# Kernel optimization log

Measured on AMD Instinct MI355X. Metric: run time of the kernel, lower is better.

## Reference

```python
import jax, jax.numpy as jnp
import numpy as np

N, H, DDE, NH = 256, 256, 64, 4

def setup_inputs() -> dict:
    key = jax.random.key(0)
    ks = jax.random.split(key, 12)
    rn = lambda k, s, sc=1.0: (jax.random.normal(k, s) * sc).astype(jnp.float32)
    return {
        "action_hidden_state": rn(ks[0], (N, H)),
        "goal_hidden_state": rn(ks[1], (N, H)),
        "goal": rn(ks[2], (N, 2)),
        "action": rn(ks[3], (N, 2)),
        "W_dist": rn(ks[4], (8, DDE), 0.3),          # distEmbedding Linear(8, dde)
        "b_dist": jnp.zeros((DDE,), jnp.float32),
        "W_gate": rn(ks[5], (DDE, H), 0.1),          # gateFC Linear(dde, H)
        "b_gate": jnp.zeros((H,), jnp.float32),
        "w": rn(ks[6], (NH, 1, H, H), 0.06),         # GAT per-head projection
        "a": rn(ks[7], (1, 1, 2 * H, 1), 0.06),      # attention vector
        "bias": jnp.zeros((H,), jnp.float32),
    }

def reference(action_hidden_state, goal_hidden_state, goal, action,
              W_dist, b_dist, W_gate, b_gate, w, a, bias):
    n = goal.shape[0]
    # --- InteractionGate.cal_gate: x1[i,j] = x[j], x2[i,j] = x[i] ---
    g1 = jnp.broadcast_to(goal[None, :, :], (n, n, 2))
    g2 = jnp.broadcast_to(goal[:, None, :], (n, n, 2))
    a1 = jnp.broadcast_to(action[None, :, :], (n, n, 2))
    a2 = jnp.broadcast_to(action[:, None, :], (n, n, 2))
    dist = jnp.concatenate([a2, g2, a1, g1], axis=-1)                 # [n,n,8]
    gate = jax.nn.sigmoid(jax.nn.relu(dist @ W_dist + b_dist) @ W_gate + b_gate)  # [n,n,H]
    # temp_action_1[i,j] = action_hidden_state[j]
    gate_action = gate * jnp.tanh(action_hidden_state[None, :, :])    # [n,n,H]
    # diagonal entries replaced by goal_hidden_state (mask_goal = eye)
    eye = jnp.eye(n, dtype=bool)[:, :, None]
    gated_h = jnp.where(eye, goal_hidden_state[None, :, :], gate_action)  # [n,n,H]

    # --- GAT assembly: h_self[i,k] = ahs[i]; h_other = cat(ahs, gated_h) ---
    h_other = jnp.concatenate([action_hidden_state[:, None, :], gated_h], axis=1)  # [n,n+1,H]

    wm = w[:, 0]          # [NH,H,H]
    a_flat = a[0, 0, :, 0]  # [2H]
    f = wm.shape[-1]
    n_head = wm.shape[0]
    # h_self rows along k are all identical -> project once per (head, node)
    hsp = jnp.einsum('nh,zhf->znf', action_hidden_state, wm)          # [NH,n,f]
    hop = jnp.einsum('nkh,zhf->znkf', h_other, wm)                    # [NH,n,n+1,f]
    # cat([h_self', h_other']) @ a  ==  h_self'@a[:f] + h_other'@a[f:]
    score = (hsp @ a_flat[:f])[:, :, None] + hop @ a_flat[f:]         # [NH,n,n+1]
    e = jnp.where(score > 0, score, 0.2 * score)                      # LeakyReLU(0.2)
    alpha = jax.nn.softmax(e, axis=-1)                                # softmax over neighbors
    # h_attn = matmul(h_other, w) == hop; weighted sum over k, mean over heads
    out = jnp.einsum('znk,znkf->nf', alpha, hop) / n_head             # [n,f]
    return jax.nn.relu(out) + bias
```

## Files before the change

### kernel.cpp

```cpp
#include <hip/hip_runtime.h>
#include <hip/hip_bf16.h>

#define NN 256
#define HH 256

typedef __attribute__((ext_vector_type(8))) short short8;
typedef __attribute__((ext_vector_type(4))) float f32x4;

__device__ __forceinline__ ushort f2bf(float x) {
    __hip_bfloat16 h = __float2bfloat16(x);
    return *reinterpret_cast<ushort*>(&h);
}
__device__ __forceinline__ float bf2f(ushort u) {
    __hip_bfloat16 h = *reinterpret_cast<__hip_bfloat16*>(&u);
    return __bfloat162float(h);
}
__device__ __forceinline__ float fast_rcp(float x) {
    return __builtin_amdgcn_rcpf(x);
}
__device__ __forceinline__ float fast_tanh(float x) {
    float e = __expf(2.0f * x);
    return 1.0f - 2.0f * fast_rcp(e + 1.0f);
}
template <int CTRL>
__device__ __forceinline__ float dpp_add(float x) {
    int y = __builtin_amdgcn_update_dpp(0, __float_as_int(x), CTRL, 0xF, 0xF, true);
    return x + __int_as_float(y);
}
template <int CTRL>
__device__ __forceinline__ float dpp_max(float x) {
    int y = __builtin_amdgcn_update_dpp(0, __float_as_int(x), CTRL, 0xF, 0xF, true);
    return fmaxf(x, __int_as_float(y));
}
__device__ __forceinline__ float red16(float v) {
    v = dpp_add<0xB1>(v); v = dpp_add<0x4E>(v);
    v = dpp_add<0x141>(v); v = dpp_add<0x140>(v);
    return v;
}
__device__ __forceinline__ float red16max(float v) {
    v = dpp_max<0xB1>(v); v = dpp_max<0x4E>(v);
    v = dpp_max<0x141>(v); v = dpp_max<0x140>(v);
    return v;
}

#define WS_P   0
#define WS_Q   16384
#define WS_T   32768
#define WS_WA  98304
#define WS_WB  99328
#define WS_WGT 100352
#define WS_PV  108544
#define WS_ML  632832
#define WS_W2H 636928
#define WS_W2L 768000

__global__ __launch_bounds__(256) void precompute_kernel(
    const float* __restrict__ ahs, const float* __restrict__ goal,
    const float* __restrict__ action, const float* __restrict__ Wd,
    const float* __restrict__ b_dist, const float* __restrict__ Wg,
    const float* __restrict__ w, const float* __restrict__ a,
    float* __restrict__ ws)
{
    const int b = blockIdx.x;
    const int t = threadIdx.x;
    const int wid  = t >> 6;
    const int lane = t & 63;
    float* P  = ws + WS_P;
    float* Q  = ws + WS_Q;
    float* T  = ws + WS_T;
    float* WA = ws + WS_WA;
    float* WB = ws + WS_WB;
    ushort* WgT  = (ushort*)(ws + WS_WGT);
    ushort* W2hi = (ushort*)(ws + WS_W2H);
    ushort* W2lo = (ushort*)(ws + WS_W2L);

    __shared__ __align__(16) float tile[64][65];

    if (b < 16) {
        const int z  = b >> 2;
        const int rg = b & 3;
        const int hbase = rg*64 + wid*16;
        const f32x4 aB = *(const f32x4*)(a + lane*4);
        const f32x4 aA = *(const f32x4*)(a + HH + lane*4);
#pragma unroll 4
        for (int rr = 0; rr < 16; ++rr) {
            const int h = hbase + rr;
            const f32x4 w4 = *(const f32x4*)(w + z*HH*HH + h*HH + lane*4);
            float dA = w4.x*aA.x + w4.y*aA.y + w4.z*aA.z + w4.w*aA.w;
            float dB = w4.x*aB.x + w4.y*aB.y + w4.z*aB.z + w4.w*aB.w;
#pragma unroll
            for (int off = 32; off; off >>= 1) {
                dA += __shfl_xor(dA, off);
                dB += __shfl_xor(dB, off);
            }
            if (lane == 0) { WA[z*HH + h] = dA; WB[z*HH + h] = dB; }
        }
    } else if (b < 80) {
        const int idx = b - 16;
        const int k0  = (idx >> 2) * 64;
        const int f0  = (idx & 3) * 64;
        const int ff  = t & 63;
#pragma unroll 4
        for (int i = 0; i < 16; ++i) {
            const int kk = i*4 + wid;
            tile[kk][ff] = w[(k0 + kk)*HH + f0 + ff];
        }
        __syncthreads();
#pragma unroll 4
        for (int i = 0; i < 16; ++i) {
            const int fl = i*4 + wid;
            float x = tile[ff][fl];
            ushort hi = f2bf(x);
            ushort lo = f2bf(x - bf2f(hi));
            W2hi[(size_t)(f0 + fl)*1024 + k0 + ff] = hi;
            W2lo[(size_t)(f0 + fl)*1024 + k0 + ff] = lo;
        }
    } else if (b < 144) {
        const int i = (b - 80)*4 + wid;
        const int d = lane;
        float a0 = action[2*i], a1 = action[2*i+1];
        float g0 = goal[2*i],   g1 = goal[2*i+1];
        P[i*64 + d] = a0*Wd[0*64+d] + a1*Wd[1*64+d]
                    + g0*Wd[2*64+d] + g1*Wd[3*64+d] + b_dist[d];
        Q[i*64 + d] = a0*Wd[4*64+d] + a1*Wd[5*64+d]
                    + g0*Wd[6*64+d] + g1*Wd[7*64+d];
    } else if (b < 208) {
        const int d = b - 144;
        WgT[t*64 + d] = f2bf(Wg[d*HH + t]);
    } else {
        const int idx = ((b - 208)*256 + t)*4;
        float4 v = *(const float4*)(ahs + idx);
        float4 o;
        o.x = fast_tanh(v.x); o.y = fast_tanh(v.y);
        o.z = fast_tanh(v.z); o.w = fast_tanh(v.w);
        *(float4*)(T + idx) = o;
    }
}

__global__ __launch_bounds__(256, 2) void gat_partial_kernel(
    const float* __restrict__ ahs, const float* __restrict__ ghs,
    const float* __restrict__ b_gate, float* __restrict__ ws)
{
    const int n    = blockIdx.x >> 1;
    const int hh   = blockIdx.x & 1;
    const int t    = threadIdx.x;
    const int wid  = t >> 6;
    const int lane = t & 63;
    const int quad = lane >> 4;
    const int l15  = lane & 15;
    const int zg   = quad;
    const int jj   = l15;
    const int n0   = wid * 64;

    const float* P  = ws + WS_P;
    const float* Q  = ws + WS_Q;
    const float* T  = ws + WS_T;
    const float* WA = ws + WS_WA;
    const float* WB = ws + WS_WB;
    const ushort* WgT = (const ushort*)(ws + WS_WGT);
    float* PV = ws + WS_PV;
    float* ML = ws + WS_ML;

    __shared__ __align__(16) float part[2][4][16][4];
    __shared__ __align__(16) float alpha_w[4][16][4];
    __shared__ __align__(16) float vred[16][260];
    __shared__ __align__(16) ushort A_l[128*64];

    int hcol[4];
#pragma unroll
    for (int nt = 0; nt < 4; ++nt) hcol[nt] = n0 + nt*16 + l15;

    short8 bfrag[4][2];
    float  wa_reg[4][4];
    float  bgv[4], gval[4];
#pragma unroll
    for (int nt = 0; nt < 4; ++nt) {
#pragma unroll
        for (int kh = 0; kh < 2; ++kh)
            bfrag[nt][kh] = *(const short8*)(WgT + hcol[nt]*64 + kh*32 + quad*8);
#pragma unroll
        for (int z = 0; z < 4; ++z) wa_reg[z][nt] = WA[z*HH + hcol[nt]];
        bgv[nt]  = b_gate[hcol[nt]];
        gval[nt] = ghs[n*HH + hcol[nt]];
    }

    {
        const int jl = t >> 1;
        const int kh = t & 1;
        const float* prow = P + n*64 + kh*32;
        const float* qrow = Q + (hh*128 + jl)*64 + kh*32;
        ushort hv[32];
#pragma unroll
        for (int c = 0; c < 8; ++c) {
            f32x4 pq = *(const f32x4*)(prow + c*4);
            f32x4 qq = *(const f32x4*)(qrow + c*4);
            hv[c*4+0] = f2bf(fmaxf(pq.x + qq.x, 0.f));
            hv[c*4+1] = f2bf(fmaxf(pq.y + qq.y, 0.f));
            hv[c*4+2] = f2bf(fmaxf(pq.z + qq.z, 0.f));
            hv[c*4+3] = f2bf(fmaxf(pq.w + qq.w, 0.f));
        }
        char* rb = (char*)A_l + jl*128;
        const int sw = (jl & 7) << 4;
#pragma unroll
        for (int c2 = 0; c2 < 4; ++c2) {
            const int off = (kh*64 + c2*16) ^ sw;
            *(short8*)(rb + off) = *(const short8*)(hv + c2*8);
        }
    }

    float vacc[4][4];
    {
        float av[4];
#pragma unroll
        for (int nt = 0; nt < 4; ++nt) av[nt] = ahs[n*HH + hcol[nt]];
#pragma unroll
        for (int z = 0; z < 4; ++z)
#pragma unroll
            for (int nt = 0; nt < 4; ++nt)
                vacc[z][nt] = (hh == 0 && quad == 0) ? av[nt] : 0.f;
    }

    float cz_r, m_r, l_r;
    {
        float pc = 0.f, ps = 0.f;
        const int hb = jj*16;
#pragma unroll
        for (int i4 = 0; i4 < 4; ++i4) {
            f32x4 av = *(const f32x4*)(ahs + n*HH + hb + i4*4);
            f32x4 wb = *(const f32x4*)(WB + zg*HH + hb + i4*4);
            f32x4 wa = *(const f32x4*)(WA + zg*HH + hb + i4*4);
            pc = fmaf(av.x, wb.x, pc); pc = fmaf(av.y, wb.y, pc);
            pc = fmaf(av.z, wb.z, pc); pc = fmaf(av.w, wb.w, pc);
            ps = fmaf(av.x, wa.x, ps); ps = fmaf(av.y, wa.y, ps);
            ps = fmaf(av.z, wa.z, ps); ps = fmaf(av.w, wa.w, ps);
        }
        pc = red16(pc); ps = red16(ps);
        cz_r = pc;
        if (hh == 0) {
            float sc = pc + ps;
            m_r = sc > 0.f ? sc : 0.2f * sc;
            l_r = 1.0f;
        } else {
            m_r = -__builtin_inff();
            l_r = 0.0f;
        }
    }

    __syncthreads();

    float tval[4][4];
    {
        const int j0 = hh*128;
#pragma unroll
        for (int r = 0; r < 4; ++r) {
            const int jg = j0 + quad*4 + r;
#pragma unroll
            for (int nt = 0; nt < 4; ++nt)
                tval[nt][r] = T[jg*HH + hcol[nt]];
        }
    }

    for (int cc = 0; cc < 8; ++cc) {
        const int j0  = hh*128 + cc*16;
        const int par = cc & 1;

        const int jl = cc*16 + l15;
        const char* rb = (const char*)A_l + jl*128;
        const int sw = (l15 & 7) << 4;
        short8 afrag0 = *(const short8*)(rb + ((quad*16) ^ sw));
        short8 afrag1 = *(const short8*)(rb + ((64 + quad*16) ^ sw));

        f32x4 acc[4];
#pragma unroll
        for (int nt = 0; nt < 4; ++nt) {
            f32x4 a4 = (f32x4){0.f,0.f,0.f,0.f};
            a4 = __builtin_amdgcn_mfma_f32_16x16x32_bf16(afrag0, bfrag[nt][0], a4, 0, 0, 0);
            a4 = __builtin_amdgcn_mfma_f32_16x16x32_bf16(afrag1, bfrag[nt][1], a4, 0, 0, 0);
            acc[nt] = a4;
        }

        float vals[4][4];
#pragma unroll
        for (int r = 0; r < 4; ++r) {
            const int jg = j0 + quad*4 + r;
            const bool diag = (jg == n);
#pragma unroll
            for (int nt = 0; nt < 4; ++nt) {
                float u = acc[nt][r] + bgv[nt];
                float g = fast_rcp(1.0f + __expf(-u));
                vals[nt][r] = diag ? gval[nt] : g * tval[nt][r];
            }
        }

#pragma unroll
        for (int z = 0; z < 4; ++z) {
            float pp[4];
#pragma unroll
            for (int r = 0; r < 4; ++r) {
                float s = 0.f;
#pragma unroll
                for (int nt = 0; nt < 4; ++nt)
                    s = fmaf(vals[nt][r], wa_reg[z][nt], s);
                pp[r] = red16(s);
            }
            if (l15 == z) {
#pragma unroll
                for (int r = 0; r < 4; ++r)
                    part[par][z][quad*4 + r][wid] = pp[r];
            }
        }
        __syncthreads();

        float tnext[4][4];
        if (cc < 7) {
            const int j1 = j0 + 16;
#pragma unroll
            for (int r = 0; r < 4; ++r) {
                const int jg = j1 + quad*4 + r;
#pragma unroll
                for (int nt = 0; nt < 4; ++nt)
                    tnext[nt][r] = T[jg*HH + hcol[nt]];
            }
        }

        float scl0, scl1, scl2, scl3;
        {
            f32x4 pr = *(const f32x4*)&part[par][zg][jj][0];
            float s = cz_r + ((pr.x + pr.y) + (pr.z + pr.w));
            float e = s > 0.f ? s : 0.2f * s;
            float mx = red16max(e);
            float m_new = fmaxf(m_r, mx);
            float at = __expf(e - m_new);
            float ss = red16(at);
            float scale = __expf(m_r - m_new);
            l_r = l_r * scale + ss;
            m_r = m_new;
            alpha_w[wid][jj][zg] = at;
            scl0 = __shfl(scale, 0);
            scl1 = __shfl(scale, 16);
            scl2 = __shfl(scale, 32);
            scl3 = __shfl(scale, 48);
        }
#pragma unroll
        for (int nt = 0; nt < 4; ++nt) {
            vacc[0][nt] *= scl0; vacc[1][nt] *= scl1;
            vacc[2][nt] *= scl2; vacc[3][nt] *= scl3;
        }
#pragma unroll
        for (int r = 0; r < 4; ++r) {
            f32x4 al = *(const f32x4*)&alpha_w[wid][quad*4 + r][0];
#pragma unroll
            for (int nt = 0; nt < 4; ++nt) {
                float v = vals[nt][r];
                vacc[0][nt] = fmaf(al.x, v, vacc[0][nt]);
                vacc[1][nt] = fmaf(al.y, v, vacc[1][nt]);
                vacc[2][nt] = fmaf(al.z, v, vacc[2][nt]);
                vacc[3][nt] = fmaf(al.w, v, vacc[3][nt]);
            }
        }
        if (cc < 7) {
#pragma unroll
            for (int nt = 0; nt < 4; ++nt)
#pragma unroll
                for (int r = 0; r < 4; ++r)
                    tval[nt][r] = tnext[nt][r];
        }
    }

#pragma unroll
    for (int z = 0; z < 4; ++z)
#pragma unroll
        for (int nt = 0; nt < 4; ++nt)
            vred[quad*4 + z][hcol[nt]] = vacc[z][nt];
    __syncthreads();
#pragma unroll
    for (int z = 0; z < 4; ++z) {
        float s = (vred[0*4+z][t] + vred[1*4+z][t]) + (vred[2*4+z][t] + vred[3*4+z][t]);
        PV[((size_t)(hh*4 + z)*NN + n)*HH + t] = s;
    }
    if (wid == 0 && l15 == 0) {
        ML[((hh*4 + zg)*NN + n)*2 + 0] = m_r;
        ML[((hh*4 + zg)*NN + n)*2 + 1] = l_r;
    }
}

__global__ __launch_bounds__(256) void gat_out_kernel(
    const float* __restrict__ bias, const float* __restrict__ ws,
    float* __restrict__ out)
{
    const int n0 = (blockIdx.x >> 4) * 16;
    const int f0 = (blockIdx.x & 15) * 16;
    const int t    = threadIdx.x;
    const int wid  = t >> 6;
    const int lane = t & 63;
    const int quad = lane >> 4;
    const int l15  = lane & 15;

    const float* PV = ws + WS_PV;
    const float* ML = ws + WS_ML;
    const ushort* W2hi = (const ushort*)(ws + WS_W2H);
    const ushort* W2lo = (const ushort*)(ws + WS_W2L);

    __shared__ __align__(16) float redc[3][16][17];
    __shared__ __align__(16) float sq[16][4][2];

    if (t < 128) {
        const int n_i = t >> 3, z = (t >> 1) & 3, q = t & 1;
        float m = ML[((q*4 + z)*NN + n0 + n_i)*2 + 0];
        float l = ML[((q*4 + z)*NN + n0 + n_i)*2 + 1];
        float mm = fmaxf(m, __shfl_xor(m, 1));
        float s  = __expf(m - mm);
        float ls = l * s;
        ls += __shfl_xor(ls, 1);
        sq[n_i][z][q] = s * fast_rcp(ls);
    }
    __syncthreads();

    f32x4 acc = (f32x4){0.f,0.f,0.f,0.f};

    const float s0 = sq[l15][wid][0];
    const float s1 = sq[l15][wid][1];
    const float* pv0 = PV + ((size_t)(0*4 + wid)*NN + n0 + l15)*HH;
    const float* pv1 = PV + ((size_t)(1*4 + wid)*NN + n0 + l15)*HH;

    for (int ks = 0; ks < 8; ++ks) {
        const int kp = ks*32 + quad*8;
        f32x4 p0a = *(const f32x4*)(pv0 + kp);
        f32x4 p0b = *(const f32x4*)(pv0 + kp + 4);
        f32x4 p1a = *(const f32x4*)(pv1 + kp);
        f32x4 p1b = *(const f32x4*)(pv1 + kp + 4);
        float v[8];
        v[0] = s0*p0a.x + s1*p1a.x; v[1] = s0*p0a.y + s1*p1a.y;
        v[2] = s0*p0a.z + s1*p1a.z; v[3] = s0*p0a.w + s1*p1a.w;
        v[4] = s0*p0b.x + s1*p1b.x; v[5] = s0*p0b.y + s1*p1b.y;
        v[6] = s0*p0b.z + s1*p1b.z; v[7] = s0*p0b.w + s1*p1b.w;
        ushort hi[8], lo[8];
#pragma unroll
        for (int c = 0; c < 8; ++c) {
            hi[c] = f2bf(v[c]);
            lo[c] = f2bf(v[c] - bf2f(hi[c]));
        }
        short8 ah = *(short8*)hi;
        short8 al = *(short8*)lo;
        const size_t boff = (size_t)(f0 + l15)*1024 + wid*256 + kp;
        short8 bh = *(const short8*)(W2hi + boff);
        short8 bl = *(const short8*)(W2lo + boff);
        acc = __builtin_amdgcn_mfma_f32_16x16x32_bf16(ah, bh, acc, 0, 0, 0);
        acc = __builtin_amdgcn_mfma_f32_16x16x32_bf16(ah, bl, acc, 0, 0, 0);
        acc = __builtin_amdgcn_mfma_f32_16x16x32_bf16(al, bh, acc, 0, 0, 0);
    }

    if (wid > 0) {
#pragma unroll
        for (int r = 0; r < 4; ++r)
            redc[wid-1][quad*4 + r][l15] = acc[r];
    }
    __syncthreads();
    if (wid == 0) {
        const int f = f0 + l15;
        float bv = bias[f];
#pragma unroll
        for (int r = 0; r < 4; ++r) {
            const int row = quad*4 + r;
            float s = acc[r]
                    + redc[0][row][l15]
                    + redc[1][row][l15]
                    + redc[2][row][l15];
            out[(size_t)(n0 + row)*HH + f] = fmaxf(0.25f * s, 0.f) + bv;
        }
    }
}

extern "C" void kernel_launch(void* const* d_in, const int* in_sizes, int n_in,
                              void* d_out, int out_size, void* d_ws, size_t ws_size,
                              hipStream_t stream)
{
    const float* ahs    = (const float*)d_in[0];
    const float* ghs    = (const float*)d_in[1];
    const float* goal   = (const float*)d_in[2];
    const float* action = (const float*)d_in[3];
    const float* Wd     = (const float*)d_in[4];
    const float* b_dist = (const float*)d_in[5];
    const float* Wg     = (const float*)d_in[6];
    const float* b_gate = (const float*)d_in[7];
    const float* w      = (const float*)d_in[8];
    const float* a      = (const float*)d_in[9];
    const float* bias   = (const float*)d_in[10];
    float* ws   = (float*)d_ws;
    float* outp = (float*)d_out;

    precompute_kernel<<<272, 256, 0, stream>>>(ahs, goal, action, Wd, b_dist, Wg, w, a, ws);
    gat_partial_kernel<<<512, 256, 0, stream>>>(ahs, ghs, b_gate, ws);
    gat_out_kernel<<<256, 256, 0, stream>>>(bias, ws, outp);
}
```

Measured before the change: 114.6 us.

## Split GAT partial work into four neighbor quarters per node

Each node's neighbor range is now split into four blocks of 64 instead of two blocks of 128, doubling the grid to 1024 blocks and raising the launch-bounds occupancy hint to 4. The output kernel merges four partial softmax states (max/sum) and four partial PV sums instead of two. The aim is more parallelism and better latency hiding across the MI355X CUs. In exchange the workspace for partial PV doubles, the output kernel reads twice as much partial data, and the higher occupancy target may force register spilling.

```diff
diff --git a/kernel.cpp b/kernel.cpp
--- a/kernel.cpp
+++ b/kernel.cpp
@@ -50,9 +50,9 @@
 #define WS_WB  99328
 #define WS_WGT 100352
 #define WS_PV  108544
-#define WS_ML  632832
-#define WS_W2H 636928
-#define WS_W2L 768000
+#define WS_ML  1157120
+#define WS_W2H 1165312
+#define WS_W2L 1296384
 
 __global__ __launch_bounds__(256) void precompute_kernel(
     const float* __restrict__ ahs, const float* __restrict__ goal,
@@ -137,12 +137,12 @@
     }
 }
 
-__global__ __launch_bounds__(256, 2) void gat_partial_kernel(
+__global__ __launch_bounds__(256, 4) void gat_partial_kernel(
     const float* __restrict__ ahs, const float* __restrict__ ghs,
     const float* __restrict__ b_gate, float* __restrict__ ws)
 {
-    const int n    = blockIdx.x >> 1;
-    const int hh   = blockIdx.x & 1;
+    const int n    = blockIdx.x >> 2;
+    const int qq   = blockIdx.x & 3;
     const int t    = threadIdx.x;
     const int wid  = t >> 6;
     const int lane = t & 63;
@@ -164,7 +164,7 @@
     __shared__ __align__(16) float part[2][4][16][4];
     __shared__ __align__(16) float alpha_w[4][16][4];
     __shared__ __align__(16) float vred[16][260];
-    __shared__ __align__(16) ushort A_l[128*64];
+    __shared__ __align__(16) ushort A_l[64*64];
 
     int hcol[4];
 #pragma unroll
@@ -185,25 +185,25 @@
     }
 
     {
-        const int jl = t >> 1;
-        const int kh = t & 1;
-        const float* prow = P + n*64 + kh*32;
-        const float* qrow = Q + (hh*128 + jl)*64 + kh*32;
-        ushort hv[32];
-#pragma unroll
-        for (int c = 0; c < 8; ++c) {
+        const int jl   = t >> 2;
+        const int kseg = t & 3;
+        const float* prow = P + n*64 + kseg*16;
+        const float* qrow = Q + (qq*64 + jl)*64 + kseg*16;
+        ushort hv[16];
+#pragma unroll
+        for (int c = 0; c < 4; ++c) {
             f32x4 pq = *(const f32x4*)(prow + c*4);
-            f32x4 qq = *(const f32x4*)(qrow + c*4);
-            hv[c*4+0] = f2bf(fmaxf(pq.x + qq.x, 0.f));
-            hv[c*4+1] = f2bf(fmaxf(pq.y + qq.y, 0.f));
-            hv[c*4+2] = f2bf(fmaxf(pq.z + qq.z, 0.f));
-            hv[c*4+3] = f2bf(fmaxf(pq.w + qq.w, 0.f));
+            f32x4 qv = *(const f32x4*)(qrow + c*4);
+            hv[c*4+0] = f2bf(fmaxf(pq.x + qv.x, 0.f));
+            hv[c*4+1] = f2bf(fmaxf(pq.y + qv.y, 0.f));
+            hv[c*4+2] = f2bf(fmaxf(pq.z + qv.z, 0.f));
+            hv[c*4+3] = f2bf(fmaxf(pq.w + qv.w, 0.f));
         }
         char* rb = (char*)A_l + jl*128;
         const int sw = (jl & 7) << 4;
 #pragma unroll
-        for (int c2 = 0; c2 < 4; ++c2) {
-            const int off = (kh*64 + c2*16) ^ sw;
+        for (int c2 = 0; c2 < 2; ++c2) {
+            const int off = (kseg*32 + c2*16) ^ sw;
             *(short8*)(rb + off) = *(const short8*)(hv + c2*8);
         }
     }
@@ -217,7 +217,7 @@
         for (int z = 0; z < 4; ++z)
 #pragma unroll
             for (int nt = 0; nt < 4; ++nt)
-                vacc[z][nt] = (hh == 0 && quad == 0) ? av[nt] : 0.f;
+                vacc[z][nt] = (qq == 0 && quad == 0) ? av[nt] : 0.f;
     }
 
     float cz_r, m_r, l_r;
@@ -236,7 +236,7 @@
         }
         pc = red16(pc); ps = red16(ps);
         cz_r = pc;
-        if (hh == 0) {
+        if (qq == 0) {
             float sc = pc + ps;
             m_r = sc > 0.f ? sc : 0.2f * sc;
             l_r = 1.0f;
@@ -250,7 +250,7 @@
 
     float tval[4][4];
     {
-        const int j0 = hh*128;
+        const int j0 = qq*64;
 #pragma unroll
         for (int r = 0; r < 4; ++r) {
             const int jg = j0 + quad*4 + r;
@@ -260,8 +260,8 @@
         }
     }
 
-    for (int cc = 0; cc < 8; ++cc) {
-        const int j0  = hh*128 + cc*16;
+    for (int cc = 0; cc < 4; ++cc) {
+        const int j0  = qq*64 + cc*16;
         const int par = cc & 1;
 
         const int jl = cc*16 + l15;
@@ -312,7 +312,7 @@
         __syncthreads();
 
         float tnext[4][4];
-        if (cc < 7) {
+        if (cc < 3) {
             const int j1 = j0 + 16;
 #pragma unroll
             for (int r = 0; r < 4; ++r) {
@@ -358,7 +358,7 @@
                 vacc[3][nt] = fmaf(al.w, v, vacc[3][nt]);
             }
         }
-        if (cc < 7) {
+        if (cc < 3) {
 #pragma unroll
             for (int nt = 0; nt < 4; ++nt)
 #pragma unroll
@@ -376,11 +376,11 @@
 #pragma unroll
     for (int z = 0; z < 4; ++z) {
         float s = (vred[0*4+z][t] + vred[1*4+z][t]) + (vred[2*4+z][t] + vred[3*4+z][t]);
-        PV[((size_t)(hh*4 + z)*NN + n)*HH + t] = s;
+        PV[((size_t)(qq*4 + z)*NN + n)*HH + t] = s;
     }
     if (wid == 0 && l15 == 0) {
-        ML[((hh*4 + zg)*NN + n)*2 + 0] = m_r;
-        ML[((hh*4 + zg)*NN + n)*2 + 1] = l_r;
+        ML[((qq*4 + zg)*NN + n)*2 + 0] = m_r;
+        ML[((qq*4 + zg)*NN + n)*2 + 1] = l_r;
     }
 }
 
@@ -402,38 +402,50 @@
     const ushort* W2lo = (const ushort*)(ws + WS_W2L);
 
     __shared__ __align__(16) float redc[3][16][17];
-    __shared__ __align__(16) float sq[16][4][2];
-
-    if (t < 128) {
-        const int n_i = t >> 3, z = (t >> 1) & 3, q = t & 1;
+    __shared__ __align__(16) float sq[16][4][4];
+
+    {
+        const int n_i = t >> 4, z = (t >> 2) & 3, q = t & 3;
         float m = ML[((q*4 + z)*NN + n0 + n_i)*2 + 0];
         float l = ML[((q*4 + z)*NN + n0 + n_i)*2 + 1];
         float mm = fmaxf(m, __shfl_xor(m, 1));
+        mm = fmaxf(mm, __shfl_xor(mm, 2));
         float s  = __expf(m - mm);
         float ls = l * s;
         ls += __shfl_xor(ls, 1);
+        ls += __shfl_xor(ls, 2);
         sq[n_i][z][q] = s * fast_rcp(ls);
     }
     __syncthreads();
 
     f32x4 acc = (f32x4){0.f,0.f,0.f,0.f};
 
-    const float s0 = sq[l15][wid][0];
-    const float s1 = sq[l15][wid][1];
-    const float* pv0 = PV + ((size_t)(0*4 + wid)*NN + n0 + l15)*HH;
-    const float* pv1 = PV + ((size_t)(1*4 + wid)*NN + n0 + l15)*HH;
+    float sc[4];
+#pragma unroll
+    for (int q = 0; q < 4; ++q) sc[q] = sq[l15][wid][q];
+    const float* pv[4];
+#pragma unroll
+    for (int q = 0; q < 4; ++q)
+        pv[q] = PV + ((size_t)(q*4 + wid)*NN + n0 + l15)*HH;
 
     for (int ks = 0; ks < 8; ++ks) {
         const int kp = ks*32 + quad*8;
-        f32x4 p0a = *(const f32x4*)(pv0 + kp);
-        f32x4 p0b = *(const f32x4*)(pv0 + kp + 4);
-        f32x4 p1a = *(const f32x4*)(pv1 + kp);
-        f32x4 p1b = *(const f32x4*)(pv1 + kp + 4);
         float v[8];
-        v[0] = s0*p0a.x + s1*p1a.x; v[1] = s0*p0a.y + s1*p1a.y;
-        v[2] = s0*p0a.z + s1*p1a.z; v[3] = s0*p0a.w + s1*p1a.w;
-        v[4] = s0*p0b.x + s1*p1b.x; v[5] = s0*p0b.y + s1*p1b.y;
-        v[6] = s0*p0b.z + s1*p1b.z; v[7] = s0*p0b.w + s1*p1b.w;
+        {
+            f32x4 pa = *(const f32x4*)(pv[0] + kp);
+            f32x4 pb = *(const f32x4*)(pv[0] + kp + 4);
+            v[0] = sc[0]*pa.x; v[1] = sc[0]*pa.y; v[2] = sc[0]*pa.z; v[3] = sc[0]*pa.w;
+            v[4] = sc[0]*pb.x; v[5] = sc[0]*pb.y; v[6] = sc[0]*pb.z; v[7] = sc[0]*pb.w;
+        }
+#pragma unroll
+        for (int q = 1; q < 4; ++q) {
+            f32x4 pa = *(const f32x4*)(pv[q] + kp);
+            f32x4 pb = *(const f32x4*)(pv[q] + kp + 4);
+            v[0] = fmaf(sc[q], pa.x, v[0]); v[1] = fmaf(sc[q], pa.y, v[1]);
+            v[2] = fmaf(sc[q], pa.z, v[2]); v[3] = fmaf(sc[q], pa.w, v[3]);
+            v[4] = fmaf(sc[q], pb.x, v[4]); v[5] = fmaf(sc[q], pb.y, v[5]);
+            v[6] = fmaf(sc[q], pb.z, v[6]); v[7] = fmaf(sc[q], pb.w, v[7]);
+        }
         ushort hi[8], lo[8];
 #pragma unroll
         for (int c = 0; c < 8; ++c) {
@@ -490,6 +502,6 @@
     float* outp = (float*)d_out;
 
     precompute_kernel<<<272, 256, 0, stream>>>(ahs, goal, action, Wd, b_dist, Wg, w, a, ws);
-    gat_partial_kernel<<<512, 256, 0, stream>>>(ahs, ghs, b_gate, ws);
+    gat_partial_kernel<<<1024, 256, 0, stream>>>(ahs, ghs, b_gate, ws);
     gat_out_kernel<<<256, 256, 0, stream>>>(bias, ws, outp);
 }
```

After: 182.1 us. 1.59x slower.

## Fuse partial and output kernels into one per-row GAT kernel

Applied to the files above, without the earlier changes.

Merges the two-block-per-row partial kernel and the separate output-projection kernel into a single 512-thread kernel per node row. The two halves of the neighbour set merge their softmax state and weighted sums in shared memory, then apply the head projection with fp32 FMAs reading w directly. This drops the PV/ML workspace round trip, one launch, and the bf16 hi/lo split of w in precompute. In exchange, each block streams the full 1 MB w through a scalar FMA loop instead of using MFMA, and only 256 blocks are launched.

```diff
diff --git a/kernel.cpp b/kernel.cpp
--- a/kernel.cpp
+++ b/kernel.cpp
@@ -10,10 +10,6 @@
 __device__ __forceinline__ ushort f2bf(float x) {
     __hip_bfloat16 h = __float2bfloat16(x);
     return *reinterpret_cast<ushort*>(&h);
-}
-__device__ __forceinline__ float bf2f(ushort u) {
-    __hip_bfloat16 h = *reinterpret_cast<__hip_bfloat16*>(&u);
-    return __bfloat162float(h);
 }
 __device__ __forceinline__ float fast_rcp(float x) {
     return __builtin_amdgcn_rcpf(x);
@@ -49,10 +45,6 @@
 #define WS_WA  98304
 #define WS_WB  99328
 #define WS_WGT 100352
-#define WS_PV  108544
-#define WS_ML  632832
-#define WS_W2H 636928
-#define WS_W2L 768000
 
 __global__ __launch_bounds__(256) void precompute_kernel(
     const float* __restrict__ ahs, const float* __restrict__ goal,
@@ -70,11 +62,7 @@
     float* T  = ws + WS_T;
     float* WA = ws + WS_WA;
     float* WB = ws + WS_WB;
-    ushort* WgT  = (ushort*)(ws + WS_WGT);
-    ushort* W2hi = (ushort*)(ws + WS_W2H);
-    ushort* W2lo = (ushort*)(ws + WS_W2L);
-
-    __shared__ __align__(16) float tile[64][65];
+    ushort* WgT = (ushort*)(ws + WS_WGT);
 
     if (b < 16) {
         const int z  = b >> 2;
@@ -96,27 +84,7 @@
             if (lane == 0) { WA[z*HH + h] = dA; WB[z*HH + h] = dB; }
         }
     } else if (b < 80) {
-        const int idx = b - 16;
-        const int k0  = (idx >> 2) * 64;
-        const int f0  = (idx & 3) * 64;
-        const int ff  = t & 63;
-#pragma unroll 4
-        for (int i = 0; i < 16; ++i) {
-            const int kk = i*4 + wid;
-            tile[kk][ff] = w[(k0 + kk)*HH + f0 + ff];
-        }
-        __syncthreads();
-#pragma unroll 4
-        for (int i = 0; i < 16; ++i) {
-            const int fl = i*4 + wid;
-            float x = tile[ff][fl];
-            ushort hi = f2bf(x);
-            ushort lo = f2bf(x - bf2f(hi));
-            W2hi[(size_t)(f0 + fl)*1024 + k0 + ff] = hi;
-            W2lo[(size_t)(f0 + fl)*1024 + k0 + ff] = lo;
-        }
-    } else if (b < 144) {
-        const int i = (b - 80)*4 + wid;
+        const int i = (b - 16)*4 + wid;
         const int d = lane;
         float a0 = action[2*i], a1 = action[2*i+1];
         float g0 = goal[2*i],   g1 = goal[2*i+1];
@@ -124,11 +92,11 @@
                     + g0*Wd[2*64+d] + g1*Wd[3*64+d] + b_dist[d];
         Q[i*64 + d] = a0*Wd[4*64+d] + a1*Wd[5*64+d]
                     + g0*Wd[6*64+d] + g1*Wd[7*64+d];
-    } else if (b < 208) {
-        const int d = b - 144;
+    } else if (b < 144) {
+        const int d = b - 80;
         WgT[t*64 + d] = f2bf(Wg[d*HH + t]);
     } else {
-        const int idx = ((b - 208)*256 + t)*4;
+        const int idx = ((b - 144)*256 + t)*4;
         float4 v = *(const float4*)(ahs + idx);
         float4 o;
         o.x = fast_tanh(v.x); o.y = fast_tanh(v.y);
@@ -137,14 +105,17 @@
     }
 }
 
-__global__ __launch_bounds__(256, 2) void gat_partial_kernel(
+__global__ __launch_bounds__(512, 2) void gat_row_kernel(
     const float* __restrict__ ahs, const float* __restrict__ ghs,
-    const float* __restrict__ b_gate, float* __restrict__ ws)
+    const float* __restrict__ b_gate, const float* __restrict__ bias,
+    const float* __restrict__ w, const float* __restrict__ ws,
+    float* __restrict__ out)
 {
-    const int n    = blockIdx.x >> 1;
-    const int hh   = blockIdx.x & 1;
+    const int n    = blockIdx.x;
     const int t    = threadIdx.x;
-    const int wid  = t >> 6;
+    const int wid4 = t >> 6;
+    const int hh   = wid4 >> 2;
+    const int wid  = wid4 & 3;
     const int lane = t & 63;
     const int quad = lane >> 4;
     const int l15  = lane & 15;
@@ -158,13 +129,14 @@
     const float* WA = ws + WS_WA;
     const float* WB = ws + WS_WB;
     const ushort* WgT = (const ushort*)(ws + WS_WGT);
-    float* PV = ws + WS_PV;
-    float* ML = ws + WS_ML;
-
-    __shared__ __align__(16) float part[2][4][16][4];
-    __shared__ __align__(16) float alpha_w[4][16][4];
+
+    __shared__ __align__(16) float part[2][2][4][16][4];
+    __shared__ __align__(16) float alpha_w[2][4][16][4];
     __shared__ __align__(16) float vred[16][260];
-    __shared__ __align__(16) ushort A_l[128*64];
+    __shared__ __align__(16) float ml[2][4][2];
+    __shared__ __align__(16) float merged[4][256];
+    __shared__ __align__(16) float proj[2][256];
+    __shared__ __align__(16) ushort A_l[256*64];
 
     int hcol[4];
 #pragma unroll
@@ -188,7 +160,7 @@
         const int jl = t >> 1;
         const int kh = t & 1;
         const float* prow = P + n*64 + kh*32;
-        const float* qrow = Q + (hh*128 + jl)*64 + kh*32;
+        const float* qrow = Q + jl*64 + kh*32;
         ushort hv[32];
 #pragma unroll
         for (int c = 0; c < 8; ++c) {
@@ -264,7 +236,7 @@
         const int j0  = hh*128 + cc*16;
         const int par = cc & 1;
 
-        const int jl = cc*16 + l15;
+        const int jl = j0 + l15;
         const char* rb = (const char*)A_l + jl*128;
         const int sw = (l15 & 7) << 4;
         short8 afrag0 = *(const short8*)(rb + ((quad*16) ^ sw));
@@ -306,7 +278,7 @@
             if (l15 == z) {
 #pragma unroll
                 for (int r = 0; r < 4; ++r)
-                    part[par][z][quad*4 + r][wid] = pp[r];
+                    part[hh][par][z][quad*4 + r][wid] = pp[r];
             }
         }
         __syncthreads();
@@ -325,7 +297,7 @@
 
         float scl0, scl1, scl2, scl3;
         {
-            f32x4 pr = *(const f32x4*)&part[par][zg][jj][0];
+            f32x4 pr = *(const f32x4*)&part[hh][par][zg][jj][0];
             float s = cz_r + ((pr.x + pr.y) + (pr.z + pr.w));
             float e = s > 0.f ? s : 0.2f * s;
             float mx = red16max(e);
@@ -335,7 +307,7 @@
             float scale = __expf(m_r - m_new);
             l_r = l_r * scale + ss;
             m_r = m_new;
-            alpha_w[wid][jj][zg] = at;
+            alpha_w[hh][wid][jj][zg] = at;
             scl0 = __shfl(scale, 0);
             scl1 = __shfl(scale, 16);
             scl2 = __shfl(scale, 32);
@@ -348,7 +320,7 @@
         }
 #pragma unroll
         for (int r = 0; r < 4; ++r) {
-            f32x4 al = *(const f32x4*)&alpha_w[wid][quad*4 + r][0];
+            f32x4 al = *(const f32x4*)&alpha_w[hh][wid][quad*4 + r][0];
 #pragma unroll
             for (int nt = 0; nt < 4; ++nt) {
                 float v = vals[nt][r];
@@ -367,107 +339,66 @@
         }
     }
 
-#pragma unroll
-    for (int z = 0; z < 4; ++z)
-#pragma unroll
-        for (int nt = 0; nt < 4; ++nt)
-            vred[quad*4 + z][hcol[nt]] = vacc[z][nt];
-    __syncthreads();
+    if (wid == 0 && l15 == 0) {
+        ml[hh][zg][0] = m_r;
+        ml[hh][zg][1] = l_r;
+    }
+    __syncthreads();
+
+    float shz[4];
 #pragma unroll
     for (int z = 0; z < 4; ++z) {
-        float s = (vred[0*4+z][t] + vred[1*4+z][t]) + (vred[2*4+z][t] + vred[3*4+z][t]);
-        PV[((size_t)(hh*4 + z)*NN + n)*HH + t] = s;
-    }
-    if (wid == 0 && l15 == 0) {
-        ML[((hh*4 + zg)*NN + n)*2 + 0] = m_r;
-        ML[((hh*4 + zg)*NN + n)*2 + 1] = l_r;
-    }
-}
-
-__global__ __launch_bounds__(256) void gat_out_kernel(
-    const float* __restrict__ bias, const float* __restrict__ ws,
-    float* __restrict__ out)
-{
-    const int n0 = (blockIdx.x >> 4) * 16;
-    const int f0 = (blockIdx.x & 15) * 16;
-    const int t    = threadIdx.x;
-    const int wid  = t >> 6;
-    const int lane = t & 63;
-    const int quad = lane >> 4;
-    const int l15  = lane & 15;
-
-    const float* PV = ws + WS_PV;
-    const float* ML = ws + WS_ML;
-    const ushort* W2hi = (const ushort*)(ws + WS_W2H);
-    const ushort* W2lo = (const ushort*)(ws + WS_W2L);
-
-    __shared__ __align__(16) float redc[3][16][17];
-    __shared__ __align__(16) float sq[16][4][2];
-
-    if (t < 128) {
-        const int n_i = t >> 3, z = (t >> 1) & 3, q = t & 1;
-        float m = ML[((q*4 + z)*NN + n0 + n_i)*2 + 0];
-        float l = ML[((q*4 + z)*NN + n0 + n_i)*2 + 1];
-        float mm = fmaxf(m, __shfl_xor(m, 1));
-        float s  = __expf(m - mm);
-        float ls = l * s;
-        ls += __shfl_xor(ls, 1);
-        sq[n_i][z][q] = s * fast_rcp(ls);
-    }
-    __syncthreads();
-
-    f32x4 acc = (f32x4){0.f,0.f,0.f,0.f};
-
-    const float s0 = sq[l15][wid][0];
-    const float s1 = sq[l15][wid][1];
-    const float* pv0 = PV + ((size_t)(0*4 + wid)*NN + n0 + l15)*HH;
-    const float* pv1 = PV + ((size_t)(1*4 + wid)*NN + n0 + l15)*HH;
-
-    for (int ks = 0; ks < 8; ++ks) {
-        const int kp = ks*32 + quad*8;
-        f32x4 p0a = *(const f32x4*)(pv0 + kp);
-        f32x4 p0b = *(const f32x4*)(pv0 + kp + 4);
-        f32x4 p1a = *(const f32x4*)(pv1 + kp);
-        f32x4 p1b = *(const f32x4*)(pv1 + kp + 4);
-        float v[8];
-        v[0] = s0*p0a.x + s1*p1a.x; v[1] = s0*p0a.y + s1*p1a.y;
-        v[2] = s0*p0a.z + s1*p1a.z; v[3] = s0*p0a.w + s1*p1a.w;
-        v[4] = s0*p0b.x + s1*p1b.x; v[5] = s0*p0b.y + s1*p1b.y;
-        v[6] = s0*p0b.z + s1*p1b.z; v[7] = s0*p0b.w + s1*p1b.w;
-        ushort hi[8], lo[8];
-#pragma unroll
-        for (int c = 0; c < 8; ++c) {
-            hi[c] = f2bf(v[c]);
-            lo[c] = f2bf(v[c] - bf2f(hi[c]));
-        }
-        short8 ah = *(short8*)hi;
-        short8 al = *(short8*)lo;
-        const size_t boff = (size_t)(f0 + l15)*1024 + wid*256 + kp;
-        short8 bh = *(const short8*)(W2hi + boff);
-        short8 bl = *(const short8*)(W2lo + boff);
-        acc = __builtin_amdgcn_mfma_f32_16x16x32_bf16(ah, bh, acc, 0, 0, 0);
-        acc = __builtin_amdgcn_mfma_f32_16x16x32_bf16(ah, bl, acc, 0, 0, 0);
-        acc = __builtin_amdgcn_mfma_f32_16x16x32_bf16(al, bh, acc, 0, 0, 0);
-    }
-
-    if (wid > 0) {
-#pragma unroll
-        for (int r = 0; r < 4; ++r)
-            redc[wid-1][quad*4 + r][l15] = acc[r];
-    }
-    __syncthreads();
-    if (wid == 0) {
-        const int f = f0 + l15;
-        float bv = bias[f];
-#pragma unroll
-        for (int r = 0; r < 4; ++r) {
-            const int row = quad*4 + r;
-            float s = acc[r]
-                    + redc[0][row][l15]
-                    + redc[1][row][l15]
-                    + redc[2][row][l15];
-            out[(size_t)(n0 + row)*HH + f] = fmaxf(0.25f * s, 0.f) + bv;
-        }
+        float m0 = ml[0][z][0], l0 = ml[0][z][1];
+        float m1 = ml[1][z][0], l1 = ml[1][z][1];
+        float M  = fmaxf(m0, m1);
+        float e0 = __expf(m0 - M), e1 = __expf(m1 - M);
+        float L  = l0*e0 + l1*e1;
+        shz[z] = (hh == 0 ? e0 : e1) * fast_rcp(L);
+    }
+
+    if (hh == 0) {
+#pragma unroll
+        for (int z = 0; z < 4; ++z)
+#pragma unroll
+            for (int nt = 0; nt < 4; ++nt)
+                vred[quad*4 + z][hcol[nt]] = shz[z] * vacc[z][nt];
+    }
+    __syncthreads();
+    if (hh == 1) {
+#pragma unroll
+        for (int z = 0; z < 4; ++z)
+#pragma unroll
+            for (int nt = 0; nt < 4; ++nt)
+                vred[quad*4 + z][hcol[nt]] += shz[z] * vacc[z][nt];
+    }
+    __syncthreads();
+
+    if (t < 256) {
+#pragma unroll
+        for (int z = 0; z < 4; ++z)
+            merged[z][t] = (vred[0*4+z][t] + vred[1*4+z][t])
+                         + (vred[2*4+z][t] + vred[3*4+z][t]);
+    }
+    __syncthreads();
+
+    {
+        const int fP = t & 255;
+        const int zh = t >> 8;
+        const float* w0 = w + (size_t)(zh*2 + 0)*HH*HH + fP;
+        const float* w1 = w + (size_t)(zh*2 + 1)*HH*HH + fP;
+        const float* m0p = &merged[zh*2 + 0][0];
+        const float* m1p = &merged[zh*2 + 1][0];
+        float ac0 = 0.f, ac1 = 0.f;
+#pragma unroll 8
+        for (int h = 0; h < 256; ++h) {
+            ac0 = fmaf(m0p[h], w0[(size_t)h*HH], ac0);
+            ac1 = fmaf(m1p[h], w1[(size_t)h*HH], ac1);
+        }
+        proj[zh][fP] = ac0 + ac1;
+    }
+    __syncthreads();
+    if (t < 256) {
+        out[(size_t)n*HH + t] = fmaxf(0.25f * (proj[0][t] + proj[1][t]), 0.f) + bias[t];
     }
 }
 
@@ -489,7 +420,6 @@
     float* ws   = (float*)d_ws;
     float* outp = (float*)d_out;
 
-    precompute_kernel<<<272, 256, 0, stream>>>(ahs, goal, action, Wd, b_dist, Wg, w, a, ws);
-    gat_partial_kernel<<<512, 256, 0, stream>>>(ahs, ghs, b_gate, ws);
-    gat_out_kernel<<<256, 256, 0, stream>>>(bias, ws, outp);
-}
+    precompute_kernel<<<208, 256, 0, stream>>>(ahs, goal, action, Wd, b_dist, Wg, w, a, ws);
+    gat_row_kernel<<<256, 512, 0, stream>>>(ahs, ghs, b_gate, bias, w, ws, outp);
+}
```

New measurement: 118.2 us. +3.2%, slower.
